# Kernel tuning notes

Measured on AMD Instinct MI355X. Metric: run time of the kernel, lower is better.

## Reference

```python
import jax, jax.numpy as jnp
import numpy as np

IN_FEATURES = 4096
OUT_FEATURES = 14336
BATCH = 2
SEQ = 2048
INT4_ZERO = 8  # stored uint-style int4 values in [0,16); signed value = q - 8


def setup_inputs() -> dict:
    key = jax.random.key(0)
    k_x, k_w, k_s, k_b = jax.random.split(key, 4)
    x = jax.random.normal(k_x, (BATCH, SEQ, IN_FEATURES), dtype=jnp.float32)
    weight_q = jax.random.randint(k_w, (OUT_FEATURES, IN_FEATURES), 0, 16, dtype=jnp.int32)
    weight_scale = jax.random.uniform(k_s, (OUT_FEATURES, 1), dtype=jnp.float32)
    bias = jax.random.normal(k_b, (OUT_FEATURES,), dtype=jnp.float32)
    return {"x": x, "weight_q": weight_q, "weight_scale": weight_scale, "bias": bias}


def reference(x, weight_q, weight_scale, bias):
    orig_shape = x.shape
    x2d = x.reshape(-1, orig_shape[-1])  # [T, in]
    # fused int4 dequant + matmul + bias: w = (q - zero) * per-row scale
    w = (weight_q.astype(x.dtype) - INT4_ZERO) * weight_scale  # [out, in]
    y2d = jnp.einsum('ti,oi->to', x2d, w) + bias  # [T, out]
    return y2d.reshape(*orig_shape[:-1], w.shape[0])
```

## Files before the change

kernel.cpp:

```cpp
#include <hip/hip_runtime.h>
#include <hip/hip_bf16.h>


#define AS1 __attribute__((address_space(1)))
#define AS3 __attribute__((address_space(3)))

typedef __attribute__((ext_vector_type(8))) short short8;
typedef __attribute__((ext_vector_type(4))) float f32x4;

static constexpr int IN_F   = 4096;
static constexpr int OUT_F  = 14336;
static constexpr int TOKENS = 2 * 2048;


__device__ __forceinline__ unsigned short bf16_rne(float f) {
    unsigned int u = __float_as_uint(f);
    u += 0x7fffu + ((u >> 16) & 1u);
    return (unsigned short)(u >> 16);
}

__global__ void convert_x_kernel(const float4* __restrict__ x,
                                 ushort4* __restrict__ xb) {
    size_t i = (size_t)blockIdx.x * blockDim.x + threadIdx.x;
    float4 v = x[i];
    ushort4 r;
    r.x = bf16_rne(v.x); r.y = bf16_rne(v.y);
    r.z = bf16_rne(v.z); r.w = bf16_rne(v.w);
    xb[i] = r;
}

__global__ void convert_w_kernel(const int4* __restrict__ q,
                                 ushort4* __restrict__ wb) {
    size_t i = (size_t)blockIdx.x * blockDim.x + threadIdx.x;
    int4 v = q[i];
    ushort4 r;
    r.x = (unsigned short)(__float_as_uint((float)(v.x - 8)) >> 16);
    r.y = (unsigned short)(__float_as_uint((float)(v.y - 8)) >> 16);
    r.z = (unsigned short)(__float_as_uint((float)(v.z - 8)) >> 16);
    r.w = (unsigned short)(__float_as_uint((float)(v.w - 8)) >> 16);
    wb[i] = r;
}


__global__ __launch_bounds__(256)
void gemm_bt_kernel(const unsigned short* __restrict__ A,
                    const unsigned short* __restrict__ B,
                    const float* __restrict__ scale,
                    const float* __restrict__ bias,
                    float* __restrict__ C) {
    constexpr int K  = IN_F;
    constexpr int N  = OUT_F;
    constexpr int BM = 128, BN = 128, BK = 32;

    __shared__ __align__(16) unsigned short sA[BM * BK];
    __shared__ __align__(16) unsigned short sB[BN * BK];

    const int tid  = threadIdx.x;
    const int wave = tid >> 6;
    const int lane = tid & 63;
    const int l16  = lane & 15;
    const int lq   = lane >> 4;

    const int mBase = blockIdx.y * BM;
    const int nBase = blockIdx.x * BN;
    const int wm = (wave >> 1) * 64;
    const int wn = (wave & 1) * 64;

    const int sr = tid >> 2;
    const int sc = (tid & 3) * 8;

    const unsigned short* gA = A + (size_t)(mBase + sr) * K + sc;
    const unsigned short* gB = B + (size_t)(nBase + sr) * K + sc;
    unsigned short* lA = &sA[sr * BK + sc];
    unsigned short* lB = &sB[sr * BK + sc];

    f32x4 acc[4][4] = {};

    for (int k0 = 0; k0 < K; k0 += BK) {
        __builtin_amdgcn_global_load_lds((const AS1 void*)(gA + k0),
                                         (AS3 void*)lA, 16, 0, 0);
        __builtin_amdgcn_global_load_lds((const AS1 void*)(gA + (size_t)64 * K + k0),
                                         (AS3 void*)(lA + 64 * BK), 16, 0, 0);
        __builtin_amdgcn_global_load_lds((const AS1 void*)(gB + k0),
                                         (AS3 void*)lB, 16, 0, 0);
        __builtin_amdgcn_global_load_lds((const AS1 void*)(gB + (size_t)64 * K + k0),
                                         (AS3 void*)(lB + 64 * BK), 16, 0, 0);
        __syncthreads();

        short8 af[4], bfr[4];
#pragma unroll
        for (int i = 0; i < 4; ++i)
            af[i] = *(const short8*)&sA[(wm + i * 16 + l16) * BK + lq * 8];
#pragma unroll
        for (int j = 0; j < 4; ++j)
            bfr[j] = *(const short8*)&sB[(wn + j * 16 + l16) * BK + lq * 8];

#pragma unroll
        for (int i = 0; i < 4; ++i)
#pragma unroll
            for (int j = 0; j < 4; ++j)
                acc[i][j] = __builtin_amdgcn_mfma_f32_16x16x32_bf16(
                    af[i], bfr[j], acc[i][j], 0, 0, 0);
        __syncthreads();
    }

#pragma unroll
    for (int j = 0; j < 4; ++j) {
        const int n = nBase + wn + j * 16 + l16;
        const float s  = scale[n];
        const float bb = bias[n];
#pragma unroll
        for (int i = 0; i < 4; ++i) {
            const int m0 = mBase + wm + i * 16 + lq * 4;
#pragma unroll
            for (int r = 0; r < 4; ++r)
                C[(size_t)(m0 + r) * N + n] = acc[i][j][r] * s + bb;
        }
    }
}


extern "C" void kernel_launch(void* const* d_in, const int* in_sizes, int n_in,
                              void* d_out, int out_size, void* d_ws, size_t ws_size,
                              hipStream_t stream) {
    const float* x      = (const float*)d_in[0];
    const int*   wq     = (const int*)d_in[1];
    const float* wscale = (const float*)d_in[2];
    const float* wbias  = (const float*)d_in[3];
    float* out = (float*)d_out;

    unsigned short* wbf = (unsigned short*)d_ws;
    unsigned short* xbf = wbf + (size_t)OUT_F * IN_F;

    convert_w_kernel<<<57344, 256, 0, stream>>>((const int4*)wq, (ushort4*)wbf);
    convert_x_kernel<<<16384, 256, 0, stream>>>((const float4*)x, (ushort4*)xbf);

    dim3 grid(OUT_F / 128, TOKENS / 128);
    gemm_bt_kernel<<<grid, 256, 0, stream>>>(xbf, wbf, wscale, wbias, out);
}
```

Baseline: 954.7 us.

## Double GEMM K-tile to 64 with XOR-swizzled LDS and batch conversion loads

The GEMM K-tile grows from 32 to 64, which halves the number of load/sync iterations, and the LDS layout gets an XOR swizzle on 16-byte chunks to avoid bank conflicts on fragment reads. The conversion kernels each handle four vectors per thread with a quarter of the blocks, which gives more memory-level parallelism per thread. LDS use doubles to 32KB per block, which may reduce occupancy.

After: 1.027 ms. 1.08x slower.

```diff
diff --git a/kernel.cpp b/kernel.cpp
--- a/kernel.cpp
+++ b/kernel.cpp
@@ -19,26 +19,48 @@
     return (unsigned short)(u >> 16);
 }
 
-__global__ void convert_x_kernel(const float4* __restrict__ x,
-                                 ushort4* __restrict__ xb) {
-    size_t i = (size_t)blockIdx.x * blockDim.x + threadIdx.x;
-    float4 v = x[i];
-    ushort4 r;
-    r.x = bf16_rne(v.x); r.y = bf16_rne(v.y);
-    r.z = bf16_rne(v.z); r.w = bf16_rne(v.w);
-    xb[i] = r;
-}
-
-__global__ void convert_w_kernel(const int4* __restrict__ q,
-                                 ushort4* __restrict__ wb) {
-    size_t i = (size_t)blockIdx.x * blockDim.x + threadIdx.x;
-    int4 v = q[i];
+__device__ __forceinline__ ushort4 cvt_w4(int4 v) {
     ushort4 r;
     r.x = (unsigned short)(__float_as_uint((float)(v.x - 8)) >> 16);
     r.y = (unsigned short)(__float_as_uint((float)(v.y - 8)) >> 16);
     r.z = (unsigned short)(__float_as_uint((float)(v.z - 8)) >> 16);
     r.w = (unsigned short)(__float_as_uint((float)(v.w - 8)) >> 16);
-    wb[i] = r;
+    return r;
+}
+
+__device__ __forceinline__ ushort4 cvt_x4(float4 v) {
+    ushort4 r;
+    r.x = bf16_rne(v.x); r.y = bf16_rne(v.y);
+    r.z = bf16_rne(v.z); r.w = bf16_rne(v.w);
+    return r;
+}
+
+__global__ void convert_w_kernel(const int4* __restrict__ q,
+                                 ushort4* __restrict__ wb) {
+    const size_t G = (size_t)14336 * 256;
+    size_t i = (size_t)blockIdx.x * blockDim.x + threadIdx.x;
+    int4 v0 = q[i];
+    int4 v1 = q[i + G];
+    int4 v2 = q[i + 2 * G];
+    int4 v3 = q[i + 3 * G];
+    wb[i]         = cvt_w4(v0);
+    wb[i + G]     = cvt_w4(v1);
+    wb[i + 2 * G] = cvt_w4(v2);
+    wb[i + 3 * G] = cvt_w4(v3);
+}
+
+__global__ void convert_x_kernel(const float4* __restrict__ x,
+                                 ushort4* __restrict__ xb) {
+    const size_t G = (size_t)4096 * 256;
+    size_t i = (size_t)blockIdx.x * blockDim.x + threadIdx.x;
+    float4 v0 = x[i];
+    float4 v1 = x[i + G];
+    float4 v2 = x[i + 2 * G];
+    float4 v3 = x[i + 3 * G];
+    xb[i]         = cvt_x4(v0);
+    xb[i + G]     = cvt_x4(v1);
+    xb[i + 2 * G] = cvt_x4(v2);
+    xb[i + 3 * G] = cvt_x4(v3);
 }
 
 
@@ -50,10 +72,10 @@
                     float* __restrict__ C) {
     constexpr int K  = IN_F;
     constexpr int N  = OUT_F;
-    constexpr int BM = 128, BN = 128, BK = 32;
+    constexpr int BK = 64;
 
-    __shared__ __align__(16) unsigned short sA[BM * BK];
-    __shared__ __align__(16) unsigned short sB[BN * BK];
+    __shared__ __align__(16) unsigned short sA[128 * BK];
+    __shared__ __align__(16) unsigned short sB[128 * BK];
 
     const int tid  = threadIdx.x;
     const int wave = tid >> 6;
@@ -61,46 +83,55 @@
     const int l16  = lane & 15;
     const int lq   = lane >> 4;
 
-    const int mBase = blockIdx.y * BM;
-    const int nBase = blockIdx.x * BN;
+    const int mBase = blockIdx.y * 128;
+    const int nBase = blockIdx.x * 128;
     const int wm = (wave >> 1) * 64;
     const int wn = (wave & 1) * 64;
 
-    const int sr = tid >> 2;
-    const int sc = (tid & 3) * 8;
+    int srow[4], soff[4];
+#pragma unroll
+    for (int c = 0; c < 4; ++c) {
+        const int s = c * 256 + tid;
+        srow[c] = s >> 3;
+        soff[c] = (((s & 7) ^ (srow[c] & 7)) * 8);
+    }
 
-    const unsigned short* gA = A + (size_t)(mBase + sr) * K + sc;
-    const unsigned short* gB = B + (size_t)(nBase + sr) * K + sc;
-    unsigned short* lA = &sA[sr * BK + sc];
-    unsigned short* lB = &sB[sr * BK + sc];
+    const unsigned short* gA = A + (size_t)mBase * K;
+    const unsigned short* gB = B + (size_t)nBase * K;
 
     f32x4 acc[4][4] = {};
 
     for (int k0 = 0; k0 < K; k0 += BK) {
-        __builtin_amdgcn_global_load_lds((const AS1 void*)(gA + k0),
-                                         (AS3 void*)lA, 16, 0, 0);
-        __builtin_amdgcn_global_load_lds((const AS1 void*)(gA + (size_t)64 * K + k0),
-                                         (AS3 void*)(lA + 64 * BK), 16, 0, 0);
-        __builtin_amdgcn_global_load_lds((const AS1 void*)(gB + k0),
-                                         (AS3 void*)lB, 16, 0, 0);
-        __builtin_amdgcn_global_load_lds((const AS1 void*)(gB + (size_t)64 * K + k0),
-                                         (AS3 void*)(lB + 64 * BK), 16, 0, 0);
+#pragma unroll
+        for (int c = 0; c < 4; ++c) {
+            const int s = c * 256 + tid;
+            __builtin_amdgcn_global_load_lds(
+                (const AS1 void*)(gA + (size_t)srow[c] * K + k0 + soff[c]),
+                (AS3 void*)(sA + s * 8), 16, 0, 0);
+            __builtin_amdgcn_global_load_lds(
+                (const AS1 void*)(gB + (size_t)srow[c] * K + k0 + soff[c]),
+                (AS3 void*)(sB + s * 8), 16, 0, 0);
+        }
         __syncthreads();
 
-        short8 af[4], bfr[4];
 #pragma unroll
-        for (int i = 0; i < 4; ++i)
-            af[i] = *(const short8*)&sA[(wm + i * 16 + l16) * BK + lq * 8];
+        for (int h = 0; h < 2; ++h) {
+            const int xk = ((h * 4 + lq) ^ (l16 & 7)) * 8;
+            short8 af[4], bfr[4];
 #pragma unroll
-        for (int j = 0; j < 4; ++j)
-            bfr[j] = *(const short8*)&sB[(wn + j * 16 + l16) * BK + lq * 8];
+            for (int i = 0; i < 4; ++i)
+                af[i] = *(const short8*)&sA[(wm + i * 16 + l16) * BK + xk];
+#pragma unroll
+            for (int j = 0; j < 4; ++j)
+                bfr[j] = *(const short8*)&sB[(wn + j * 16 + l16) * BK + xk];
 
 #pragma unroll
-        for (int i = 0; i < 4; ++i)
+            for (int i = 0; i < 4; ++i)
 #pragma unroll
-            for (int j = 0; j < 4; ++j)
-                acc[i][j] = __builtin_amdgcn_mfma_f32_16x16x32_bf16(
-                    af[i], bfr[j], acc[i][j], 0, 0, 0);
+                for (int j = 0; j < 4; ++j)
+                    acc[i][j] = __builtin_amdgcn_mfma_f32_16x16x32_bf16(
+                        af[i], bfr[j], acc[i][j], 0, 0, 0);
+        }
         __syncthreads();
     }
 
@@ -132,8 +163,8 @@
     unsigned short* wbf = (unsigned short*)d_ws;
     unsigned short* xbf = wbf + (size_t)OUT_F * IN_F;
 
-    convert_w_kernel<<<57344, 256, 0, stream>>>((const int4*)wq, (ushort4*)wbf);
-    convert_x_kernel<<<16384, 256, 0, stream>>>((const float4*)x, (ushort4*)xbf);
+    convert_w_kernel<<<14336, 256, 0, stream>>>((const int4*)wq, (ushort4*)wbf);
+    convert_x_kernel<<<4096, 256, 0, stream>>>((const float4*)x, (ushort4*)xbf);
 
     dim3 grid(OUT_F / 128, TOKENS / 128);
     gemm_bt_kernel<<<grid, 256, 0, stream>>>(xbf, wbf, wscale, wbias, out);
```

## Switch GEMM to 32x32x16 MFMA with XOR-swizzled LDS layout

Applied to the files above, without the earlier changes.

Replaces the 4x4 grid of 16x16x32 bf16 MFMAs per wave with a 2x2 grid of 32x32x16 MFMAs, splitting each BK=32 step into two K halves. The global-to-LDS staging now uses an XOR swizzle on the 8-element column chunk keyed by row, so the fragment reads from LDS avoid bank conflicts. The aim is fewer LDS fragment loads per MFMA and conflict-free shared memory access. The epilogue is remapped to the 32x32 accumulator layout, which changes the output store pattern.

Measured after the change: 991.7 us. 3.9% more time.

```diff
diff --git a/kernel.cpp b/kernel.cpp
--- a/kernel.cpp
+++ b/kernel.cpp
@@ -6,7 +6,7 @@
 #define AS3 __attribute__((address_space(3)))
 
 typedef __attribute__((ext_vector_type(8))) short short8;
-typedef __attribute__((ext_vector_type(4))) float f32x4;
+typedef __attribute__((ext_vector_type(16))) float f32x16;
 
 static constexpr int IN_F   = 4096;
 static constexpr int OUT_F  = 14336;
@@ -50,31 +50,31 @@
                     float* __restrict__ C) {
     constexpr int K  = IN_F;
     constexpr int N  = OUT_F;
-    constexpr int BM = 128, BN = 128, BK = 32;
+    constexpr int BK = 32;
 
-    __shared__ __align__(16) unsigned short sA[BM * BK];
-    __shared__ __align__(16) unsigned short sB[BN * BK];
+    __shared__ __align__(16) unsigned short sA[128 * BK];
+    __shared__ __align__(16) unsigned short sB[128 * BK];
 
     const int tid  = threadIdx.x;
     const int wave = tid >> 6;
     const int lane = tid & 63;
-    const int l16  = lane & 15;
-    const int lq   = lane >> 4;
+    const int l31  = lane & 31;
+    const int g    = lane >> 5;
 
-    const int mBase = blockIdx.y * BM;
-    const int nBase = blockIdx.x * BN;
+    const int mBase = blockIdx.y * 128;
+    const int nBase = blockIdx.x * 128;
     const int wm = (wave >> 1) * 64;
     const int wn = (wave & 1) * 64;
 
     const int sr = tid >> 2;
-    const int sc = (tid & 3) * 8;
+    const int sc = ((tid & 3) ^ (sr & 3)) * 8;
 
     const unsigned short* gA = A + (size_t)(mBase + sr) * K + sc;
     const unsigned short* gB = B + (size_t)(nBase + sr) * K + sc;
-    unsigned short* lA = &sA[sr * BK + sc];
-    unsigned short* lB = &sB[sr * BK + sc];
+    unsigned short* lA = &sA[tid * 8];
+    unsigned short* lB = &sB[tid * 8];
 
-    f32x4 acc[4][4] = {};
+    f32x16 acc[2][2] = {};
 
     for (int k0 = 0; k0 < K; k0 += BK) {
         __builtin_amdgcn_global_load_lds((const AS1 void*)(gA + k0),
@@ -87,34 +87,43 @@
                                          (AS3 void*)(lB + 64 * BK), 16, 0, 0);
         __syncthreads();
 
-        short8 af[4], bfr[4];
 #pragma unroll
-        for (int i = 0; i < 4; ++i)
-            af[i] = *(const short8*)&sA[(wm + i * 16 + l16) * BK + lq * 8];
+        for (int h = 0; h < 2; ++h) {
+            const int q = h * 2 + g;
+            short8 af[2], bfr[2];
 #pragma unroll
-        for (int j = 0; j < 4; ++j)
-            bfr[j] = *(const short8*)&sB[(wn + j * 16 + l16) * BK + lq * 8];
-
+            for (int i = 0; i < 2; ++i) {
+                const int r = wm + i * 32 + l31;
+                af[i] = *(const short8*)&sA[r * BK + (q ^ (r & 3)) * 8];
+            }
 #pragma unroll
-        for (int i = 0; i < 4; ++i)
+            for (int j = 0; j < 2; ++j) {
+                const int r = wn + j * 32 + l31;
+                bfr[j] = *(const short8*)&sB[r * BK + (q ^ (r & 3)) * 8];
+            }
 #pragma unroll
-            for (int j = 0; j < 4; ++j)
-                acc[i][j] = __builtin_amdgcn_mfma_f32_16x16x32_bf16(
-                    af[i], bfr[j], acc[i][j], 0, 0, 0);
+            for (int i = 0; i < 2; ++i)
+#pragma unroll
+                for (int j = 0; j < 2; ++j)
+                    acc[i][j] = __builtin_amdgcn_mfma_f32_32x32x16_bf16(
+                        af[i], bfr[j], acc[i][j], 0, 0, 0);
+        }
         __syncthreads();
     }
 
 #pragma unroll
-    for (int j = 0; j < 4; ++j) {
-        const int n = nBase + wn + j * 16 + l16;
+    for (int j = 0; j < 2; ++j) {
+        const int n = nBase + wn + j * 32 + l31;
         const float s  = scale[n];
         const float bb = bias[n];
 #pragma unroll
-        for (int i = 0; i < 4; ++i) {
-            const int m0 = mBase + wm + i * 16 + lq * 4;
+        for (int i = 0; i < 2; ++i) {
+            const int m0 = mBase + wm + i * 32 + 4 * g;
 #pragma unroll
-            for (int r = 0; r < 4; ++r)
-                C[(size_t)(m0 + r) * N + n] = acc[i][j][r] * s + bb;
+            for (int reg = 0; reg < 16; ++reg) {
+                const int row = (reg & 3) + 8 * (reg >> 2);
+                C[(size_t)(m0 + row) * N + n] = acc[i][j][reg] * s + bb;
+            }
         }
     }
 }
```
